# Optimization experiments

Hardware: AMD Instinct MI355X
Metric: run time of the kernel (lower is better)

## Reference

```python
import jax, jax.numpy as jnp
import numpy as np

BN_EPS = 1e-5

def _l2norm(x, axis):
    return x / (1e-6 + jnp.linalg.norm(x, axis=axis, keepdims=True))

def setup_inputs() -> dict:
    key = jax.random.key(0)
    ks = jax.random.split(key, 4)
    c, k = 512, 64
    b, h, w = 16, 64, 64
    x = jax.random.normal(ks[0], (b, c, h, w), dtype=jnp.float32)
    conv1_w = jax.random.normal(ks[1], (c, c), dtype=jnp.float32) * np.sqrt(2.0 / c)
    conv1_b = jnp.zeros((c,), dtype=jnp.float32)
    mu = jax.random.normal(ks[2], (1, c, k), dtype=jnp.float32) * np.sqrt(2.0 / k)
    mu = _l2norm(mu, axis=1)
    conv2_w = jax.random.normal(ks[3], (c, c), dtype=jnp.float32) * np.sqrt(2.0 / c)
    bn_gamma = jnp.ones((c,), dtype=jnp.float32)
    bn_beta = jnp.zeros((c,), dtype=jnp.float32)
    bn_mean = jnp.zeros((c,), dtype=jnp.float32)
    bn_var = jnp.ones((c,), dtype=jnp.float32)
    return {"x": x, "conv1_w": conv1_w, "conv1_b": conv1_b, "mu": mu,
            "conv2_w": conv2_w, "bn_gamma": bn_gamma, "bn_beta": bn_beta,
            "bn_mean": bn_mean, "bn_var": bn_var}

STAGE_NUM = 3

def reference(x, conv1_w, conv1_b, mu, conv2_w, bn_gamma, bn_beta, bn_mean, bn_var):
    idn = x
    b, c, h, w = x.shape
    # conv1: 1x1 conv with bias
    xf = jnp.einsum('oc,bchw->bohw', conv1_w, x) + conv1_b[None, :, None, None]
    xf = xf.reshape(b, c, h * w)            # [b, c, n]
    mu_b = jnp.broadcast_to(mu, (b,) + mu.shape[1:])  # [b, c, k]

    # EM iterations (no-grad in original; here just the forward loop)
    def em_step(mu_b, _):
        z = jnp.einsum('bcn,bck->bnk', xf, mu_b)          # [b, n, k]
        z = jax.nn.softmax(z, axis=2)
        z_ = z / (1e-6 + z.sum(axis=1, keepdims=True))
        mu_new = _l2norm(jnp.einsum('bcn,bnk->bck', xf, z_), axis=1)
        return mu_new, z

    mu_b, zs = jax.lax.scan(em_step, mu_b, None, length=STAGE_NUM)
    z = zs[-1]                                            # last-stage responsibilities
    mu_b = jax.lax.stop_gradient(mu_b)
    z = jax.lax.stop_gradient(z)

    xr = jnp.einsum('bck,bnk->bcn', mu_b, z).reshape(b, c, h, w)
    xr = jax.nn.relu(xr)
    # conv2: 1x1 conv (no bias) + BatchNorm (inference mode)
    xr = jnp.einsum('oc,bchw->bohw', conv2_w, xr)
    inv = bn_gamma / jnp.sqrt(bn_var + BN_EPS)
    xr = xr * inv[None, :, None, None] + (bn_beta - bn_mean * inv)[None, :, None, None]
    return jax.nn.relu(xr + idn)
```

## Files before the change

kernel.cpp:

```cpp
#include <hip/hip_runtime.h>

typedef __bf16 bf16x8 __attribute__((ext_vector_type(8)));
typedef __bf16 bf16x4 __attribute__((ext_vector_type(4)));
typedef float f32x4 __attribute__((ext_vector_type(4)));

constexpr int CC = 512;
constexpr int KK = 64;
constexpr int NN = 4096;
constexpr int BB = 16;

constexpr size_t R1_OFF    = 0;
constexpr size_t R2_OFF    = 16777216;
constexpr size_t Z_OFF     = 33554432;
constexpr size_t ZT_OFF    = 35651584;
constexpr size_t MUACC_OFF = 37748736;
constexpr size_t ZSUM_OFF  = 38273024;
constexpr size_t MUBF_OFF  = 38274048;
constexpr size_t MUTBF_OFF = 38536192;
constexpr size_t W1BF_OFF  = 38798336;
constexpr size_t W2BF_OFF  = 38929408;

__global__ __launch_bounds__(256) void k_cvt(const float* __restrict__ src,
                                             __bf16* __restrict__ dst, int n8) {
    int i = blockIdx.x * 256 + threadIdx.x;
    if (i < n8) {
        const float4* s4 = (const float4*)src;
        float4 a = s4[i * 2], b = s4[i * 2 + 1];
        bf16x8 o;
        o[0] = (__bf16)a.x; o[1] = (__bf16)a.y; o[2] = (__bf16)a.z; o[3] = (__bf16)a.w;
        o[4] = (__bf16)b.x; o[5] = (__bf16)b.y; o[6] = (__bf16)b.z; o[7] = (__bf16)b.w;
        *(bf16x8*)&dst[(size_t)i * 8] = o;
    }
}

__global__ __launch_bounds__(256) void k_mu_bcast_bf(const float* __restrict__ mu_in,
                                                     __bf16* __restrict__ mu_bf,
                                                     __bf16* __restrict__ muT_bf) {
    int idx = blockIdx.x * 256 + threadIdx.x;
    if (idx < CC * KK) {
        int c = idx >> 6, k = idx & 63;
        __bf16 v = (__bf16)mu_in[idx];
        for (int b = 0; b < BB; ++b) {
            mu_bf[(size_t)b * CC * KK + idx] = v;
            muT_bf[((size_t)b * KK + k) * CC + c] = v;
        }
    }
}

__global__ __launch_bounds__(256) void k_xpose_cvt(const float* __restrict__ X,
                                                   __bf16* __restrict__ XT) {
    int n0 = blockIdx.x * 64, c0 = blockIdx.y * 64, b = blockIdx.z;
    __shared__ float T[64][65];
    int tid = threadIdx.x;
    const float* Xb = X + (size_t)b * CC * NN;
#pragma unroll
    for (int p = 0; p < 4; ++p) {
        int f4 = tid + p * 256;
        int row = f4 >> 4, col4 = (f4 & 15) * 4;
        float4 v = *(const float4*)&Xb[(size_t)(c0 + row) * NN + n0 + col4];
        T[row][col4 + 0] = v.x; T[row][col4 + 1] = v.y;
        T[row][col4 + 2] = v.z; T[row][col4 + 3] = v.w;
    }
    __syncthreads();
#pragma unroll
    for (int p = 0; p < 2; ++p) {
        int q = tid + p * 256;
        int nl = q >> 3, c8 = (q & 7) * 8;
        bf16x8 o;
#pragma unroll
        for (int j = 0; j < 8; ++j) o[j] = (__bf16)T[c8 + j][nl];
        *(bf16x8*)&XT[((size_t)b * NN + n0 + nl) * CC + c0 + c8] = o;
    }
}

__global__ __launch_bounds__(256) void k_conv1_mfma(
    const __bf16* __restrict__ XT, const __bf16* __restrict__ W1,
    const float* __restrict__ bias, __bf16* __restrict__ XFT,
    __bf16* __restrict__ XFC) {
    __shared__ __bf16 SM[17408];
    __shared__ float sbias[128];
    __bf16* As = SM;
    __bf16* Bs = SM + 8192;
    int tid = threadIdx.x;
    int lane = tid & 63, wave = tid >> 6;
    int wm = wave >> 1, wn = wave & 1;
    int o0 = blockIdx.x * 128, n0 = blockIdx.y * 128, b = blockIdx.z;
    const __bf16* Ab = XT + ((size_t)b * NN + n0) * CC;
    const __bf16* Bb = W1 + (size_t)o0 * CC;
    if (tid < 128) sbias[tid] = bias[o0 + tid];

    f32x4 acc[4][4];
#pragma unroll
    for (int i = 0; i < 4; ++i)
#pragma unroll
        for (int j = 0; j < 4; ++j) acc[i][j] = f32x4{0.f, 0.f, 0.f, 0.f};

    int r0 = tid >> 2, k0c = tid & 3;
    int r1 = (tid + 256) >> 2, k1c = tid & 3;
    int w0 = r0 * 32 + (k0c ^ ((r0 >> 1) & 3)) * 8;
    int w1 = r1 * 32 + (k1c ^ ((r1 >> 1) & 3)) * 8;

    bf16x8 va0, va1, vb0, vb1;
    va0 = *(const bf16x8*)(Ab + (size_t)r0 * CC + k0c * 8);
    va1 = *(const bf16x8*)(Ab + (size_t)r1 * CC + k1c * 8);
    vb0 = *(const bf16x8*)(Bb + (size_t)r0 * CC + k0c * 8);
    vb1 = *(const bf16x8*)(Bb + (size_t)r1 * CC + k1c * 8);
    *(bf16x8*)&As[w0] = va0; *(bf16x8*)&As[w1] = va1;
    *(bf16x8*)&Bs[w0] = vb0; *(bf16x8*)&Bs[w1] = vb1;
    __syncthreads();

    for (int kt = 0; kt < 16; ++kt) {
        int s = kt & 1;
        if (kt < 15) {
            const __bf16* Ak = Ab + (kt + 1) * 32;
            const __bf16* Bk = Bb + (kt + 1) * 32;
            va0 = *(const bf16x8*)(Ak + (size_t)r0 * CC + k0c * 8);
            va1 = *(const bf16x8*)(Ak + (size_t)r1 * CC + k1c * 8);
            vb0 = *(const bf16x8*)(Bk + (size_t)r0 * CC + k0c * 8);
            vb1 = *(const bf16x8*)(Bk + (size_t)r1 * CC + k1c * 8);
        }
        bf16x8 af[4], bg[4];
#pragma unroll
        for (int f = 0; f < 4; ++f) {
            int ra = wm * 64 + f * 16 + (lane & 15);
            af[f] = *(const bf16x8*)&As[s * 4096 + ra * 32 + (((lane >> 4) ^ ((ra >> 1) & 3))) * 8];
            int rb = wn * 64 + f * 16 + (lane & 15);
            bg[f] = *(const bf16x8*)&Bs[s * 4096 + rb * 32 + (((lane >> 4) ^ ((rb >> 1) & 3))) * 8];
        }
#pragma unroll
        for (int i = 0; i < 4; ++i)
#pragma unroll
            for (int j = 0; j < 4; ++j)
                acc[i][j] = __builtin_amdgcn_mfma_f32_16x16x32_bf16(af[i], bg[j], acc[i][j], 0, 0, 0);
        if (kt < 15) {
            *(bf16x8*)&As[(s ^ 1) * 4096 + w0] = va0; *(bf16x8*)&As[(s ^ 1) * 4096 + w1] = va1;
            *(bf16x8*)&Bs[(s ^ 1) * 4096 + w0] = vb0; *(bf16x8*)&Bs[(s ^ 1) * 4096 + w1] = vb1;
        }
        __syncthreads();
    }

    __bf16* TT = SM;
    int gq = lane >> 4, ln = lane & 15;
#pragma unroll
    for (int mf = 0; mf < 4; ++mf) {
#pragma unroll
        for (int nf = 0; nf < 4; ++nf) {
            int o_loc = wn * 64 + nf * 16 + ln;
            int n_loc4 = wm * 64 + mf * 16 + gq * 4;
            float bi = sbias[o_loc];
            bf16x4 oc;
#pragma unroll
            for (int r = 0; r < 4; ++r) oc[r] = (__bf16)(acc[mf][nf][r] + bi);
            *(bf16x4*)&XFC[((size_t)b * CC + o0 + o_loc) * NN + n0 + n_loc4] = oc;
#pragma unroll
            for (int r = 0; r < 4; ++r) TT[(n_loc4 + r) * 136 + o_loc] = oc[r];
        }
    }
    __syncthreads();
#pragma unroll
    for (int p = 0; p < 8; ++p) {
        int idx = tid + p * 256;
        int row = idx >> 4, ch = idx & 15;
        bf16x8 v = *(const bf16x8*)&TT[row * 136 + ch * 8];
        *(bf16x8*)&XFT[((size_t)b * NN + n0 + row) * CC + o0 + ch * 8] = v;
    }
}

__global__ __launch_bounds__(256) void k_conv2_mfma(
    const __bf16* __restrict__ W2, const __bf16* __restrict__ XRT,
    const float* __restrict__ gamma, const float* __restrict__ beta,
    const float* __restrict__ mean, const float* __restrict__ var,
    const float* __restrict__ Xres, float* __restrict__ Out) {
    __shared__ __bf16 As[2][128 * 32];
    __shared__ __bf16 Bs[2][128 * 32];
    __shared__ float sp0[128], sp1[128];
    int tid = threadIdx.x;
    int lane = tid & 63, wave = tid >> 6;
    int wm = wave >> 1, wn = wave & 1;
    int n0 = blockIdx.x * 128, m0 = blockIdx.y * 128, b = blockIdx.z;
    const __bf16* Ab = XRT + ((size_t)b * NN + n0) * CC;
    const __bf16* Bb = W2 + (size_t)m0 * CC;
    int gq = lane >> 4, ln = lane & 15;
    if (tid < 128) {
        float iv = gamma[m0 + tid] * rsqrtf(var[m0 + tid] + 1e-5f);
        sp0[tid] = iv;
        sp1[tid] = beta[m0 + tid] - mean[m0 + tid] * iv;
    }

    f32x4 xpre[4][4];
#pragma unroll
    for (int mf = 0; mf < 4; ++mf)
#pragma unroll
        for (int nf = 0; nf < 4; ++nf) {
            int o_loc = wn * 64 + nf * 16 + ln;
            int n_loc4 = wm * 64 + mf * 16 + gq * 4;
            xpre[mf][nf] = *(const f32x4*)&Xres[((size_t)b * CC + m0 + o_loc) * NN + n0 + n_loc4];
        }

    f32x4 acc[4][4];
#pragma unroll
    for (int i = 0; i < 4; ++i)
#pragma unroll
        for (int j = 0; j < 4; ++j) acc[i][j] = f32x4{0.f, 0.f, 0.f, 0.f};

    int r0 = tid >> 2, k0c = tid & 3;
    int r1 = (tid + 256) >> 2, k1c = tid & 3;
    int w0 = r0 * 32 + (k0c ^ ((r0 >> 1) & 3)) * 8;
    int w1 = r1 * 32 + (k1c ^ ((r1 >> 1) & 3)) * 8;

    bf16x8 va0, va1, vb0, vb1;
    va0 = *(const bf16x8*)(Ab + (size_t)r0 * CC + k0c * 8);
    va1 = *(const bf16x8*)(Ab + (size_t)r1 * CC + k1c * 8);
    vb0 = *(const bf16x8*)(Bb + (size_t)r0 * CC + k0c * 8);
    vb1 = *(const bf16x8*)(Bb + (size_t)r1 * CC + k1c * 8);
    *(bf16x8*)&As[0][w0] = va0; *(bf16x8*)&As[0][w1] = va1;
    *(bf16x8*)&Bs[0][w0] = vb0; *(bf16x8*)&Bs[0][w1] = vb1;
    __syncthreads();

    for (int kt = 0; kt < 16; ++kt) {
        int s = kt & 1;
        if (kt < 15) {
            const __bf16* Ak = Ab + (kt + 1) * 32;
            const __bf16* Bk = Bb + (kt + 1) * 32;
            va0 = *(const bf16x8*)(Ak + (size_t)r0 * CC + k0c * 8);
            va1 = *(const bf16x8*)(Ak + (size_t)r1 * CC + k1c * 8);
            vb0 = *(const bf16x8*)(Bk + (size_t)r0 * CC + k0c * 8);
            vb1 = *(const bf16x8*)(Bk + (size_t)r1 * CC + k1c * 8);
        }
        bf16x8 af[4], bg[4];
#pragma unroll
        for (int f = 0; f < 4; ++f) {
            int ra = wm * 64 + f * 16 + (lane & 15);
            af[f] = *(const bf16x8*)&As[s][ra * 32 + (((lane >> 4) ^ ((ra >> 1) & 3))) * 8];
            int rb = wn * 64 + f * 16 + (lane & 15);
            bg[f] = *(const bf16x8*)&Bs[s][rb * 32 + (((lane >> 4) ^ ((rb >> 1) & 3))) * 8];
        }
#pragma unroll
        for (int i = 0; i < 4; ++i)
#pragma unroll
            for (int j = 0; j < 4; ++j)
                acc[i][j] = __builtin_amdgcn_mfma_f32_16x16x32_bf16(af[i], bg[j], acc[i][j], 0, 0, 0);
        if (kt < 15) {
            *(bf16x8*)&As[s ^ 1][w0] = va0; *(bf16x8*)&As[s ^ 1][w1] = va1;
            *(bf16x8*)&Bs[s ^ 1][w0] = vb0; *(bf16x8*)&Bs[s ^ 1][w1] = vb1;
        }
        __syncthreads();
    }

#pragma unroll
    for (int mf = 0; mf < 4; ++mf) {
#pragma unroll
        for (int nf = 0; nf < 4; ++nf) {
            int o_loc = wn * 64 + nf * 16 + ln;
            int n_loc4 = wm * 64 + mf * 16 + gq * 4;
            size_t addr = ((size_t)b * CC + m0 + o_loc) * NN + n0 + n_loc4;
            float iv = sp0[o_loc], sh = sp1[o_loc];
            f32x4 xi = xpre[mf][nf];
            float4 v;
            v.x = fmaxf(acc[mf][nf][0] * iv + sh + xi[0], 0.f);
            v.y = fmaxf(acc[mf][nf][1] * iv + sh + xi[1], 0.f);
            v.z = fmaxf(acc[mf][nf][2] * iv + sh + xi[2], 0.f);
            v.w = fmaxf(acc[mf][nf][3] * iv + sh + xi[3], 0.f);
            *(float4*)&Out[addr] = v;
        }
    }
}

__global__ __launch_bounds__(256) void k_zsoftmax_mfma(
    const __bf16* __restrict__ XFT, const __bf16* __restrict__ MUT,
    __bf16* __restrict__ Z, __bf16* __restrict__ ZT, float* __restrict__ ZSUM,
    int write_z) {
    __shared__ __bf16 As[2][128 * 32];
    __shared__ __bf16 Bs[2][64 * 32];
    __shared__ __bf16 ZL[64][136];
    int tid = threadIdx.x;
    int lane = tid & 63, wave = tid >> 6;
    int n0 = blockIdx.x * 128, b = blockIdx.y;
    const __bf16* Ab = XFT + ((size_t)b * NN + n0) * CC;
    const __bf16* Bb = MUT + (size_t)b * KK * CC;

    f32x4 acc[2][4];
#pragma unroll
    for (int i = 0; i < 2; ++i)
#pragma unroll
        for (int j = 0; j < 4; ++j) acc[i][j] = f32x4{0.f, 0.f, 0.f, 0.f};

    int r0 = tid >> 2, k0c = tid & 3;
    int r1 = (tid + 256) >> 2, k1c = tid & 3;
    int w0 = r0 * 32 + (k0c ^ ((r0 >> 1) & 3)) * 8;
    int w1 = r1 * 32 + (k1c ^ ((r1 >> 1) & 3)) * 8;
    int rB = tid >> 2, kB = tid & 3;
    int wB = rB * 32 + (kB ^ ((rB >> 1) & 3)) * 8;

    bf16x8 va0, va1, vb0;
    va0 = *(const bf16x8*)(Ab + (size_t)r0 * CC + k0c * 8);
    va1 = *(const bf16x8*)(Ab + (size_t)r1 * CC + k1c * 8);
    vb0 = *(const bf16x8*)(Bb + (size_t)rB * CC + kB * 8);
    *(bf16x8*)&As[0][w0] = va0; *(bf16x8*)&As[0][w1] = va1;
    *(bf16x8*)&Bs[0][wB] = vb0;
    __syncthreads();

    for (int kt = 0; kt < 16; ++kt) {
        int s = kt & 1;
        if (kt < 15) {
            const __bf16* Ak = Ab + (kt + 1) * 32;
            const __bf16* Bk = Bb + (kt + 1) * 32;
            va0 = *(const bf16x8*)(Ak + (size_t)r0 * CC + k0c * 8);
            va1 = *(const bf16x8*)(Ak + (size_t)r1 * CC + k1c * 8);
            vb0 = *(const bf16x8*)(Bk + (size_t)rB * CC + kB * 8);
        }
        bf16x8 af[2], bg[4];
#pragma unroll
        for (int f = 0; f < 2; ++f) {
            int ra = wave * 32 + f * 16 + (lane & 15);
            af[f] = *(const bf16x8*)&As[s][ra * 32 + (((lane >> 4) ^ ((ra >> 1) & 3))) * 8];
        }
#pragma unroll
        for (int f = 0; f < 4; ++f) {
            int rb = f * 16 + (lane & 15);
            bg[f] = *(const bf16x8*)&Bs[s][rb * 32 + (((lane >> 4) ^ ((rb >> 1) & 3))) * 8];
        }
#pragma unroll
        for (int i = 0; i < 2; ++i)
#pragma unroll
            for (int j = 0; j < 4; ++j)
                acc[i][j] = __builtin_amdgcn_mfma_f32_16x16x32_bf16(af[i], bg[j], acc[i][j], 0, 0, 0);
        if (kt < 15) {
            *(bf16x8*)&As[s ^ 1][w0] = va0; *(bf16x8*)&As[s ^ 1][w1] = va1;
            *(bf16x8*)&Bs[s ^ 1][wB] = vb0;
        }
        __syncthreads();
    }

    int gq = lane >> 4, ln = lane & 15;
    float zp[4] = {0.f, 0.f, 0.f, 0.f};
#pragma unroll
    for (int mf = 0; mf < 2; ++mf) {
#pragma unroll
        for (int r = 0; r < 4; ++r) {
            float mx = fmaxf(fmaxf(acc[mf][0][r], acc[mf][1][r]),
                             fmaxf(acc[mf][2][r], acc[mf][3][r]));
            mx = fmaxf(mx, __shfl_xor(mx, 1));
            mx = fmaxf(mx, __shfl_xor(mx, 2));
            mx = fmaxf(mx, __shfl_xor(mx, 4));
            mx = fmaxf(mx, __shfl_xor(mx, 8));
            float e[4];
            float ssum = 0.f;
#pragma unroll
            for (int nf = 0; nf < 4; ++nf) { e[nf] = expf(acc[mf][nf][r] - mx); ssum += e[nf]; }
            ssum += __shfl_xor(ssum, 1);
            ssum += __shfl_xor(ssum, 2);
            ssum += __shfl_xor(ssum, 4);
            ssum += __shfl_xor(ssum, 8);
            float inv = 1.0f / ssum;
            int n_loc = wave * 32 + mf * 16 + gq * 4 + r;
#pragma unroll
            for (int nf = 0; nf < 4; ++nf) {
                float zv = e[nf] * inv;
                zp[nf] += zv;
                ZL[nf * 16 + ln][n_loc] = (__bf16)zv;
            }
        }
    }
#pragma unroll
    for (int nf = 0; nf < 4; ++nf) {
        float t = zp[nf];
        t += __shfl_xor(t, 16);
        t += __shfl_xor(t, 32);
        if (lane < 16) atomicAdd(&ZSUM[b * KK + nf * 16 + ln], t);
    }
    __syncthreads();
#pragma unroll
    for (int p = 0; p < 4; ++p) {
        int ci = tid + p * 256;
        int kr = ci >> 4, ch = (ci & 15) * 8;
        bf16x8 v = *(const bf16x8*)&ZL[kr][ch];
        *(bf16x8*)&ZT[((size_t)b * KK + kr) * NN + n0 + ch] = v;
    }
    if (write_z) {
#pragma unroll
        for (int p = 0; p < 4; ++p) {
            int idx = tid + p * 256;
            int row = idx >> 3, k8 = (idx & 7) * 8;
            bf16x8 o;
#pragma unroll
            for (int j = 0; j < 8; ++j) o[j] = ZL[k8 + j][row];
            *(bf16x8*)&Z[((size_t)b * NN + n0 + row) * KK + k8] = o;
        }
    }
}

__global__ __launch_bounds__(256) void k_muacc_mfma(
    const __bf16* __restrict__ XFC, const __bf16* __restrict__ ZT,
    float* __restrict__ MUACC) {
    __shared__ __bf16 As[2][128 * 32];
    __shared__ __bf16 Bs[2][64 * 32];
    int tid = threadIdx.x;
    int lane = tid & 63, wave = tid >> 6;
    int wm = wave >> 1, wn = wave & 1;
    int c0 = (blockIdx.x & 3) * 128, sp = blockIdx.x >> 2, b = blockIdx.y;
    size_t nbase = (size_t)sp * 512;
    const __bf16* Ab = XFC + ((size_t)b * CC + c0) * NN + nbase;
    const __bf16* Bb = ZT + (size_t)b * KK * NN + nbase;

    f32x4 acc[4][2];
#pragma unroll
    for (int i = 0; i < 4; ++i)
#pragma unroll
        for (int j = 0; j < 2; ++j) acc[i][j] = f32x4{0.f, 0.f, 0.f, 0.f};

    int r0 = tid >> 2, k0c = tid & 3;
    int r1 = (tid + 256) >> 2, k1c = tid & 3;
    int w0 = r0 * 32 + (k0c ^ ((r0 >> 1) & 3)) * 8;
    int w1 = r1 * 32 + (k1c ^ ((r1 >> 1) & 3)) * 8;
    int rB = tid >> 2, kB = tid & 3;
    int wB = rB * 32 + (kB ^ ((rB >> 1) & 3)) * 8;

    bf16x8 va0, va1, vb0;
    va0 = *(const bf16x8*)(Ab + (size_t)r0 * NN + k0c * 8);
    va1 = *(const bf16x8*)(Ab + (size_t)r1 * NN + k1c * 8);
    vb0 = *(const bf16x8*)(Bb + (size_t)rB * NN + kB * 8);
    *(bf16x8*)&As[0][w0] = va0; *(bf16x8*)&As[0][w1] = va1;
    *(bf16x8*)&Bs[0][wB] = vb0;
    __syncthreads();

    for (int kt = 0; kt < 16; ++kt) {
        int s = kt & 1;
        if (kt < 15) {
            const __bf16* Ak = Ab + (kt + 1) * 32;
            const __bf16* Bk = Bb + (kt + 1) * 32;
            va0 = *(const bf16x8*)(Ak + (size_t)r0 * NN + k0c * 8);
            va1 = *(const bf16x8*)(Ak + (size_t)r1 * NN + k1c * 8);
            vb0 = *(const bf16x8*)(Bk + (size_t)rB * NN + kB * 8);
        }
        bf16x8 af[4], bg[2];
#pragma unroll
        for (int f = 0; f < 4; ++f) {
            int ra = wm * 64 + f * 16 + (lane & 15);
            af[f] = *(const bf16x8*)&As[s][ra * 32 + (((lane >> 4) ^ ((ra >> 1) & 3))) * 8];
        }
#pragma unroll
        for (int f = 0; f < 2; ++f) {
            int rb = wn * 32 + f * 16 + (lane & 15);
            bg[f] = *(const bf16x8*)&Bs[s][rb * 32 + (((lane >> 4) ^ ((rb >> 1) & 3))) * 8];
        }
#pragma unroll
        for (int i = 0; i < 4; ++i)
#pragma unroll
            for (int j = 0; j < 2; ++j)
                acc[i][j] = __builtin_amdgcn_mfma_f32_16x16x32_bf16(af[i], bg[j], acc[i][j], 0, 0, 0);
        if (kt < 15) {
            *(bf16x8*)&As[s ^ 1][w0] = va0; *(bf16x8*)&As[s ^ 1][w1] = va1;
            *(bf16x8*)&Bs[s ^ 1][wB] = vb0;
        }
        __syncthreads();
    }

    int gq = lane >> 4, ln = lane & 15;
#pragma unroll
    for (int mf = 0; mf < 4; ++mf) {
#pragma unroll
        for (int r = 0; r < 4; ++r) {
            int row = wm * 64 + mf * 16 + gq * 4 + r;
#pragma unroll
            for (int nf = 0; nf < 2; ++nf) {
                int col = wn * 32 + nf * 16 + ln;
                atomicAdd(&MUACC[((size_t)b * CC + c0 + row) * KK + col], acc[mf][nf][r]);
            }
        }
    }
}

__global__ __launch_bounds__(64) void k_munorm_bf(
    const float* __restrict__ MUACC, const float* __restrict__ ZSUM,
    __bf16* __restrict__ mu_bf, __bf16* __restrict__ muT_bf) {
    int k = blockIdx.x;
    int b = blockIdx.y;
    int lane = threadIdx.x;
    float scale = 1.0f / (1e-6f + ZSUM[b * KK + k]);
    float v[8];
    float ss = 0.f;
#pragma unroll
    for (int i = 0; i < 8; ++i) {
        v[i] = MUACC[(size_t)b * CC * KK + (size_t)(lane + i * 64) * KK + k] * scale;
        ss += v[i] * v[i];
    }
    for (int off = 32; off; off >>= 1) ss += __shfl_xor(ss, off);
    float nrm = 1.0f / (1e-6f + sqrtf(ss));
#pragma unroll
    for (int i = 0; i < 8; ++i) {
        int c = lane + i * 64;
        __bf16 o = (__bf16)(v[i] * nrm);
        mu_bf[((size_t)b * CC + c) * KK + k] = o;
        muT_bf[((size_t)b * KK + k) * CC + c] = o;
    }
}

__global__ __launch_bounds__(256) void k_xr_mfma(
    const __bf16* __restrict__ Zm, const __bf16* __restrict__ MUB,
    __bf16* __restrict__ XRT) {
    __shared__ __bf16 SM[17408];
    __bf16* As = SM;
    __bf16* Bs = SM + 8192;
    int tid = threadIdx.x;
    int lane = tid & 63, wave = tid >> 6;
    int wm = wave >> 1, wn = wave & 1;
    int n0 = blockIdx.x * 128, c0 = blockIdx.y * 128, b = blockIdx.z;
    const __bf16* Ab = Zm + ((size_t)b * NN + n0) * KK;
    const __bf16* Bb = MUB + ((size_t)b * CC + c0) * KK;
#pragma unroll
    for (int p = 0; p < 4; ++p) {
        int idx = tid + p * 256;
        int r = idx >> 3, ch = idx & 7;
        int woff = r * 64 + ((ch ^ (r & 7)) * 8);
        *(bf16x8*)&As[woff] = *(const bf16x8*)(Ab + (size_t)r * KK + ch * 8);
        *(bf16x8*)&Bs[woff] = *(const bf16x8*)(Bb + (size_t)r * KK + ch * 8);
    }
    __syncthreads();

    f32x4 acc[4][4];
#pragma unroll
    for (int i = 0; i < 4; ++i)
#pragma unroll
        for (int j = 0; j < 4; ++j) acc[i][j] = f32x4{0.f, 0.f, 0.f, 0.f};

    int gq = lane >> 4, ln = lane & 15;
#pragma unroll
    for (int ks = 0; ks < 2; ++ks) {
        bf16x8 af[4], bg[4];
#pragma unroll
        for (int f = 0; f < 4; ++f) {
            int ra = wm * 64 + f * 16 + ln;
            af[f] = *(const bf16x8*)&As[ra * 64 + (((ks * 4 + gq) ^ (ra & 7))) * 8];
            int rb = wn * 64 + f * 16 + ln;
            bg[f] = *(const bf16x8*)&Bs[rb * 64 + (((ks * 4 + gq) ^ (rb & 7))) * 8];
        }
#pragma unroll
        for (int i = 0; i < 4; ++i)
#pragma unroll
            for (int j = 0; j < 4; ++j)
                acc[i][j] = __builtin_amdgcn_mfma_f32_16x16x32_bf16(af[i], bg[j], acc[i][j], 0, 0, 0);
    }
    __syncthreads();

    __bf16* TT = SM;
#pragma unroll
    for (int mf = 0; mf < 4; ++mf) {
#pragma unroll
        for (int nf = 0; nf < 4; ++nf) {
            int c_loc = wn * 64 + nf * 16 + ln;
            int n_loc4 = wm * 64 + mf * 16 + gq * 4;
#pragma unroll
            for (int r = 0; r < 4; ++r)
                TT[(n_loc4 + r) * 136 + c_loc] = (__bf16)fmaxf(acc[mf][nf][r], 0.f);
        }
    }
    __syncthreads();
#pragma unroll
    for (int p = 0; p < 8; ++p) {
        int idx = tid + p * 256;
        int row = idx >> 4, ch = idx & 15;
        bf16x8 v = *(const bf16x8*)&TT[row * 136 + ch * 8];
        *(bf16x8*)&XRT[((size_t)b * NN + n0 + row) * CC + c0 + ch * 8] = v;
    }
}

extern "C" void kernel_launch(void* const* d_in, const int* in_sizes, int n_in,
                              void* d_out, int out_size, void* d_ws, size_t ws_size,
                              hipStream_t stream) {
    const float* x     = (const float*)d_in[0];
    const float* w1    = (const float*)d_in[1];
    const float* b1    = (const float*)d_in[2];
    const float* mu_in = (const float*)d_in[3];
    const float* w2    = (const float*)d_in[4];
    const float* gamma = (const float*)d_in[5];
    const float* beta  = (const float*)d_in[6];
    const float* mean  = (const float*)d_in[7];
    const float* var   = (const float*)d_in[8];
    float* out = (float*)d_out;
    float* ws  = (float*)d_ws;

    __bf16* xt    = (__bf16*)(ws + R1_OFF);
    __bf16* xft   = (__bf16*)(ws + R2_OFF);
    __bf16* xrt   = (__bf16*)(ws + R2_OFF);
    __bf16* xfc   = (__bf16*)d_out;
    __bf16* zbf   = (__bf16*)(ws + Z_OFF);
    __bf16* ztbf  = (__bf16*)(ws + ZT_OFF);
    float*  muacc = ws + MUACC_OFF;
    float*  zsum  = ws + ZSUM_OFF;
    __bf16* mu_bf = (__bf16*)(ws + MUBF_OFF);
    __bf16* muT_bf= (__bf16*)(ws + MUTBF_OFF);
    __bf16* w1bf  = (__bf16*)(ws + W1BF_OFF);
    __bf16* w2bf  = (__bf16*)(ws + W2BF_OFF);

    hipLaunchKernelGGL(k_cvt, dim3(128), dim3(256), 0, stream, w1, w1bf, CC * CC / 8);
    hipLaunchKernelGGL(k_cvt, dim3(128), dim3(256), 0, stream, w2, w2bf, CC * CC / 8);
    hipLaunchKernelGGL(k_mu_bcast_bf, dim3(128), dim3(256), 0, stream, mu_in, mu_bf, muT_bf);
    hipLaunchKernelGGL(k_xpose_cvt, dim3(NN / 64, CC / 64, BB), dim3(256), 0, stream, x, xt);
    hipLaunchKernelGGL(k_conv1_mfma, dim3(CC / 128, NN / 128, BB), dim3(256), 0, stream,
                       xt, w1bf, b1, xft, xfc);
    for (int it = 0; it < 3; ++it) {
        hipMemsetAsync(muacc, 0, (size_t)(BB * CC * KK + BB * KK) * sizeof(float), stream);
        hipLaunchKernelGGL(k_zsoftmax_mfma, dim3(NN / 128, BB), dim3(256), 0, stream,
                           xft, muT_bf, zbf, ztbf, zsum, (it == 2) ? 1 : 0);
        hipLaunchKernelGGL(k_muacc_mfma, dim3(32, BB), dim3(256), 0, stream, xfc, ztbf, muacc);
        hipLaunchKernelGGL(k_munorm_bf, dim3(KK, BB), dim3(64), 0, stream, muacc, zsum,
                           mu_bf, muT_bf);
    }
    hipLaunchKernelGGL(k_xr_mfma, dim3(NN / 128, CC / 128, BB), dim3(256), 0, stream,
                       zbf, mu_bf, xrt);
    hipLaunchKernelGGL(k_conv2_mfma, dim3(NN / 128, CC / 128, BB), dim3(256), 0, stream,
                       w2bf, xrt, gamma, beta, mean, var, x, out);
}
```

Measured before the change: 430.2 us.

## Stage GEMM tiles via direct global-to-LDS loads in all MFMA kernels

```diff
diff --git a/kernel.cpp b/kernel.cpp
--- a/kernel.cpp
+++ b/kernel.cpp
@@ -19,6 +19,12 @@
 constexpr size_t MUTBF_OFF = 38536192;
 constexpr size_t W1BF_OFF  = 38798336;
 constexpr size_t W2BF_OFF  = 38929408;
+
+__device__ __forceinline__ void gload16(const void* g, void* l) {
+    __builtin_amdgcn_global_load_lds(
+        (const __attribute__((address_space(1))) void*)g,
+        (__attribute__((address_space(3))) void*)l, 16, 0, 0);
+}
 
 __global__ __launch_bounds__(256) void k_cvt(const float* __restrict__ src,
                                              __bf16* __restrict__ dst, int n8) {
@@ -95,18 +101,16 @@
 #pragma unroll
         for (int j = 0; j < 4; ++j) acc[i][j] = f32x4{0.f, 0.f, 0.f, 0.f};
 
-    int r0 = tid >> 2, k0c = tid & 3;
-    int r1 = (tid + 256) >> 2, k1c = tid & 3;
-    int w0 = r0 * 32 + (k0c ^ ((r0 >> 1) & 3)) * 8;
-    int w1 = r1 * 32 + (k1c ^ ((r1 >> 1) & 3)) * 8;
-
-    bf16x8 va0, va1, vb0, vb1;
-    va0 = *(const bf16x8*)(Ab + (size_t)r0 * CC + k0c * 8);
-    va1 = *(const bf16x8*)(Ab + (size_t)r1 * CC + k1c * 8);
-    vb0 = *(const bf16x8*)(Bb + (size_t)r0 * CC + k0c * 8);
-    vb1 = *(const bf16x8*)(Bb + (size_t)r1 * CC + k1c * 8);
-    *(bf16x8*)&As[w0] = va0; *(bf16x8*)&As[w1] = va1;
-    *(bf16x8*)&Bs[w0] = vb0; *(bf16x8*)&Bs[w1] = vb1;
+    int r0 = tid >> 2, ks0 = (tid & 3) ^ ((r0 >> 1) & 3);
+    int t1 = tid + 256;
+    int r1 = t1 >> 2, ks1 = (t1 & 3) ^ ((r1 >> 1) & 3);
+    int la0 = wave * 512;
+    int la1 = 2048 + wave * 512;
+
+    gload16(Ab + (size_t)r0 * CC + ks0 * 8, &As[la0]);
+    gload16(Ab + (size_t)r1 * CC + ks1 * 8, &As[la1]);
+    gload16(Bb + (size_t)r0 * CC + ks0 * 8, &Bs[la0]);
+    gload16(Bb + (size_t)r1 * CC + ks1 * 8, &Bs[la1]);
     __syncthreads();
 
     for (int kt = 0; kt < 16; ++kt) {
@@ -114,10 +118,11 @@
         if (kt < 15) {
             const __bf16* Ak = Ab + (kt + 1) * 32;
             const __bf16* Bk = Bb + (kt + 1) * 32;
-            va0 = *(const bf16x8*)(Ak + (size_t)r0 * CC + k0c * 8);
-            va1 = *(const bf16x8*)(Ak + (size_t)r1 * CC + k1c * 8);
-            vb0 = *(const bf16x8*)(Bk + (size_t)r0 * CC + k0c * 8);
-            vb1 = *(const bf16x8*)(Bk + (size_t)r1 * CC + k1c * 8);
+            int d = (s ^ 1) * 4096;
+            gload16(Ak + (size_t)r0 * CC + ks0 * 8, &As[d + la0]);
+            gload16(Ak + (size_t)r1 * CC + ks1 * 8, &As[d + la1]);
+            gload16(Bk + (size_t)r0 * CC + ks0 * 8, &Bs[d + la0]);
+            gload16(Bk + (size_t)r1 * CC + ks1 * 8, &Bs[d + la1]);
         }
         bf16x8 af[4], bg[4];
 #pragma unroll
@@ -132,10 +137,6 @@
 #pragma unroll
             for (int j = 0; j < 4; ++j)
                 acc[i][j] = __builtin_amdgcn_mfma_f32_16x16x32_bf16(af[i], bg[j], acc[i][j], 0, 0, 0);
-        if (kt < 15) {
-            *(bf16x8*)&As[(s ^ 1) * 4096 + w0] = va0; *(bf16x8*)&As[(s ^ 1) * 4096 + w1] = va1;
-            *(bf16x8*)&Bs[(s ^ 1) * 4096 + w0] = vb0; *(bf16x8*)&Bs[(s ^ 1) * 4096 + w1] = vb1;
-        }
         __syncthreads();
     }
 
@@ -187,6 +188,17 @@
         sp1[tid] = beta[m0 + tid] - mean[m0 + tid] * iv;
     }
 
+    int r0 = tid >> 2, ks0 = (tid & 3) ^ ((r0 >> 1) & 3);
+    int t1 = tid + 256;
+    int r1 = t1 >> 2, ks1 = (t1 & 3) ^ ((r1 >> 1) & 3);
+    int la0 = wave * 512;
+    int la1 = 2048 + wave * 512;
+
+    gload16(Ab + (size_t)r0 * CC + ks0 * 8, &As[0][la0]);
+    gload16(Ab + (size_t)r1 * CC + ks1 * 8, &As[0][la1]);
+    gload16(Bb + (size_t)r0 * CC + ks0 * 8, &Bs[0][la0]);
+    gload16(Bb + (size_t)r1 * CC + ks1 * 8, &Bs[0][la1]);
+
     f32x4 xpre[4][4];
 #pragma unroll
     for (int mf = 0; mf < 4; ++mf)
@@ -202,19 +214,6 @@
     for (int i = 0; i < 4; ++i)
 #pragma unroll
         for (int j = 0; j < 4; ++j) acc[i][j] = f32x4{0.f, 0.f, 0.f, 0.f};
-
-    int r0 = tid >> 2, k0c = tid & 3;
-    int r1 = (tid + 256) >> 2, k1c = tid & 3;
-    int w0 = r0 * 32 + (k0c ^ ((r0 >> 1) & 3)) * 8;
-    int w1 = r1 * 32 + (k1c ^ ((r1 >> 1) & 3)) * 8;
-
-    bf16x8 va0, va1, vb0, vb1;
-    va0 = *(const bf16x8*)(Ab + (size_t)r0 * CC + k0c * 8);
-    va1 = *(const bf16x8*)(Ab + (size_t)r1 * CC + k1c * 8);
-    vb0 = *(const bf16x8*)(Bb + (size_t)r0 * CC + k0c * 8);
-    vb1 = *(const bf16x8*)(Bb + (size_t)r1 * CC + k1c * 8);
-    *(bf16x8*)&As[0][w0] = va0; *(bf16x8*)&As[0][w1] = va1;
-    *(bf16x8*)&Bs[0][w0] = vb0; *(bf16x8*)&Bs[0][w1] = vb1;
     __syncthreads();
 
     for (int kt = 0; kt < 16; ++kt) {
@@ -222,10 +221,10 @@
         if (kt < 15) {
             const __bf16* Ak = Ab + (kt + 1) * 32;
             const __bf16* Bk = Bb + (kt + 1) * 32;
-            va0 = *(const bf16x8*)(Ak + (size_t)r0 * CC + k0c * 8);
-            va1 = *(const bf16x8*)(Ak + (size_t)r1 * CC + k1c * 8);
-            vb0 = *(const bf16x8*)(Bk + (size_t)r0 * CC + k0c * 8);
-            vb1 = *(const bf16x8*)(Bk + (size_t)r1 * CC + k1c * 8);
+            gload16(Ak + (size_t)r0 * CC + ks0 * 8, &As[s ^ 1][la0]);
+            gload16(Ak + (size_t)r1 * CC + ks1 * 8, &As[s ^ 1][la1]);
+            gload16(Bk + (size_t)r0 * CC + ks0 * 8, &Bs[s ^ 1][la0]);
+            gload16(Bk + (size_t)r1 * CC + ks1 * 8, &Bs[s ^ 1][la1]);
         }
         bf16x8 af[4], bg[4];
 #pragma unroll
@@ -240,10 +239,6 @@
 #pragma unroll
             for (int j = 0; j < 4; ++j)
                 acc[i][j] = __builtin_amdgcn_mfma_f32_16x16x32_bf16(af[i], bg[j], acc[i][j], 0, 0, 0);
-        if (kt < 15) {
-            *(bf16x8*)&As[s ^ 1][w0] = va0; *(bf16x8*)&As[s ^ 1][w1] = va1;
-            *(bf16x8*)&Bs[s ^ 1][w0] = vb0; *(bf16x8*)&Bs[s ^ 1][w1] = vb1;
-        }
         __syncthreads();
     }
 
@@ -285,19 +280,15 @@
 #pragma unroll
         for (int j = 0; j < 4; ++j) acc[i][j] = f32x4{0.f, 0.f, 0.f, 0.f};
 
-    int r0 = tid >> 2, k0c = tid & 3;
-    int r1 = (tid + 256) >> 2, k1c = tid & 3;
-    int w0 = r0 * 32 + (k0c ^ ((r0 >> 1) & 3)) * 8;
-    int w1 = r1 * 32 + (k1c ^ ((r1 >> 1) & 3)) * 8;
-    int rB = tid >> 2, kB = tid & 3;
-    int wB = rB * 32 + (kB ^ ((rB >> 1) & 3)) * 8;
-
-    bf16x8 va0, va1, vb0;
-    va0 = *(const bf16x8*)(Ab + (size_t)r0 * CC + k0c * 8);
-    va1 = *(const bf16x8*)(Ab + (size_t)r1 * CC + k1c * 8);
-    vb0 = *(const bf16x8*)(Bb + (size_t)rB * CC + kB * 8);
-    *(bf16x8*)&As[0][w0] = va0; *(bf16x8*)&As[0][w1] = va1;
-    *(bf16x8*)&Bs[0][wB] = vb0;
+    int r0 = tid >> 2, ks0 = (tid & 3) ^ ((r0 >> 1) & 3);
+    int t1 = tid + 256;
+    int r1 = t1 >> 2, ks1 = (t1 & 3) ^ ((r1 >> 1) & 3);
+    int la0 = wave * 512;
+    int la1 = 2048 + wave * 512;
+
+    gload16(Ab + (size_t)r0 * CC + ks0 * 8, &As[0][la0]);
+    gload16(Ab + (size_t)r1 * CC + ks1 * 8, &As[0][la1]);
+    gload16(Bb + (size_t)r0 * CC + ks0 * 8, &Bs[0][la0]);
     __syncthreads();
 
     for (int kt = 0; kt < 16; ++kt) {
@@ -305,9 +296,9 @@
         if (kt < 15) {
             const __bf16* Ak = Ab + (kt + 1) * 32;
             const __bf16* Bk = Bb + (kt + 1) * 32;
-            va0 = *(const bf16x8*)(Ak + (size_t)r0 * CC + k0c * 8);
-            va1 = *(const bf16x8*)(Ak + (size_t)r1 * CC + k1c * 8);
-            vb0 = *(const bf16x8*)(Bk + (size_t)rB * CC + kB * 8);
+            gload16(Ak + (size_t)r0 * CC + ks0 * 8, &As[s ^ 1][la0]);
+            gload16(Ak + (size_t)r1 * CC + ks1 * 8, &As[s ^ 1][la1]);
+            gload16(Bk + (size_t)r0 * CC + ks0 * 8, &Bs[s ^ 1][la0]);
         }
         bf16x8 af[2], bg[4];
 #pragma unroll
@@ -325,10 +316,6 @@
 #pragma unroll
             for (int j = 0; j < 4; ++j)
                 acc[i][j] = __builtin_amdgcn_mfma_f32_16x16x32_bf16(af[i], bg[j], acc[i][j], 0, 0, 0);
-        if (kt < 15) {
-            *(bf16x8*)&As[s ^ 1][w0] = va0; *(bf16x8*)&As[s ^ 1][w1] = va1;
-            *(bf16x8*)&Bs[s ^ 1][wB] = vb0;
-        }
         __syncthreads();
     }
 
@@ -409,19 +396,15 @@
 #pragma unroll
         for (int j = 0; j < 2; ++j) acc[i][j] = f32x4{0.f, 0.f, 0.f, 0.f};
 
-    int r0 = tid >> 2, k0c = tid & 3;
-    int r1 = (tid + 256) >> 2, k1c = tid & 3;
-    int w0 = r0 * 32 + (k0c ^ ((r0 >> 1) & 3)) * 8;
-    int w1 = r1 * 32 + (k1c ^ ((r1 >> 1) & 3)) * 8;
-    int rB = tid >> 2, kB = tid & 3;
-    int wB = rB * 32 + (kB ^ ((rB >> 1) & 3)) * 8;
-
-    bf16x8 va0, va1, vb0;
-    va0 = *(const bf16x8*)(Ab + (size_t)r0 * NN + k0c * 8);
-    va1 = *(const bf16x8*)(Ab + (size_t)r1 * NN + k1c * 8);
-    vb0 = *(const bf16x8*)(Bb + (size_t)rB * NN + kB * 8);
-    *(bf16x8*)&As[0][w0] = va0; *(bf16x8*)&As[0][w1] = va1;
-    *(bf16x8*)&Bs[0][wB] = vb0;
+    int r0 = tid >> 2, ks0 = (tid & 3) ^ ((r0 >> 1) & 3);
+    int t1 = tid + 256;
+    int r1 = t1 >> 2, ks1 = (t1 & 3) ^ ((r1 >> 1) & 3);
+    int la0 = wave * 512;
+    int la1 = 2048 + wave * 512;
+
+    gload16(Ab + (size_t)r0 * NN + ks0 * 8, &As[0][la0]);
+    gload16(Ab + (size_t)r1 * NN + ks1 * 8, &As[0][la1]);
+    gload16(Bb + (size_t)r0 * NN + ks0 * 8, &Bs[0][la0]);
     __syncthreads();
 
     for (int kt = 0; kt < 16; ++kt) {
@@ -429,9 +412,9 @@
         if (kt < 15) {
             const __bf16* Ak = Ab + (kt + 1) * 32;
             const __bf16* Bk = Bb + (kt + 1) * 32;
-            va0 = *(const bf16x8*)(Ak + (size_t)r0 * NN + k0c * 8);
-            va1 = *(const bf16x8*)(Ak + (size_t)r1 * NN + k1c * 8);
-            vb0 = *(const bf16x8*)(Bk + (size_t)rB * NN + kB * 8);
+            gload16(Ak + (size_t)r0 * NN + ks0 * 8, &As[s ^ 1][la0]);
+            gload16(Ak + (size_t)r1 * NN + ks1 * 8, &As[s ^ 1][la1]);
+            gload16(Bk + (size_t)r0 * NN + ks0 * 8, &Bs[s ^ 1][la0]);
         }
         bf16x8 af[4], bg[2];
 #pragma unroll
@@ -449,10 +432,6 @@
 #pragma unroll
             for (int j = 0; j < 2; ++j)
                 acc[i][j] = __builtin_amdgcn_mfma_f32_16x16x32_bf16(af[i], bg[j], acc[i][j], 0, 0, 0);
-        if (kt < 15) {
-            *(bf16x8*)&As[s ^ 1][w0] = va0; *(bf16x8*)&As[s ^ 1][w1] = va1;
-            *(bf16x8*)&Bs[s ^ 1][wB] = vb0;
-        }
         __syncthreads();
     }
 
@@ -510,11 +489,12 @@
     const __bf16* Bb = MUB + ((size_t)b * CC + c0) * KK;
 #pragma unroll
     for (int p = 0; p < 4; ++p) {
-        int idx = tid + p * 256;
-        int r = idx >> 3, ch = idx & 7;
-        int woff = r * 64 + ((ch ^ (r & 7)) * 8);
-        *(bf16x8*)&As[woff] = *(const bf16x8*)(Ab + (size_t)r * KK + ch * 8);
-        *(bf16x8*)&Bs[woff] = *(const bf16x8*)(Bb + (size_t)r * KK + ch * 8);
+        int cidb = p * 256 + tid;
+        int r = cidb >> 3, sx = cidb & 7;
+        int ksrc = sx ^ (r & 7);
+        int lbase = p * 2048 + wave * 512;
+        gload16(Ab + (size_t)r * KK + ksrc * 8, &As[lbase]);
+        gload16(Bb + (size_t)r * KK + ksrc * 8, &Bs[lbase]);
     }
     __syncthreads();
 
```

New measurement: 445.3 us. 1.03x slower.
